# Kernel tuning notes

Measured on AMD Instinct MI355X. Metric: run time of the kernel, lower is better.

The kernel has to match this reference:

```python
import jax, jax.numpy as jnp
import numpy as np

BATCH, T, D_MODEL = 4, 4096, 2048


def setup_inputs() -> dict:
    key = jax.random.key(0)
    kx, ka, kb, kc, kd = jax.random.split(key, 5)
    x = jax.random.normal(kx, (BATCH, T, D_MODEL), dtype=jnp.float32)
    A = jax.random.normal(ka, (D_MODEL,), dtype=jnp.float32)
    B = jax.random.normal(kb, (D_MODEL,), dtype=jnp.float32)
    C = jax.random.normal(kc, (D_MODEL,), dtype=jnp.float32)
    D = jax.random.normal(kd, (D_MODEL,), dtype=jnp.float32)
    return {"x": x, "A": A, "B": B, "C": C, "D": D}


def reference(x, A, B, C, D):
    # Diagonal LTI SSM: h_t = A*h_{t-1} + B*x_t ; y_t = C*h_t + D*x_t
    # x: (batch, T, d_model). Scan over time axis.
    batch, _, d = x.shape
    s0 = jnp.zeros((batch, d), dtype=x.dtype)

    def step(s, xt):
        s = A * s + B * xt          # (batch, d)
        yt = C * s + D * xt
        return s, yt

    # scan over leading axis -> move T to front
    _, ys = jax.lax.scan(step, s0, jnp.swapaxes(x, 0, 1))
    return jnp.swapaxes(ys, 0, 1)   # (batch, T, d_model)
```

## Files before the change

kernel.cpp:

```cpp
#include <hip/hip_runtime.h>

#define BATCHN  4
#define TLEN    4096
#define D4      512
#define DG      8
#define NDG     64
#define THREADS 512
#define TTILE   512
#define NTILE   8
#define NSUB    64
#define TSUB    8
#define TILE_F4 (TTILE * DG)

typedef float f4 __attribute__((ext_vector_type(4)));

__device__ __forceinline__ float fin(float v) {
    return fminf(fmaxf(v, -1.0e30f), 1.0e30f);
}
__device__ __forceinline__ f4 fin4(f4 v) {
    f4 r;
    r.x = fin(v.x); r.y = fin(v.y); r.z = fin(v.z); r.w = fin(v.w);
    return r;
}

struct pr { f4 p, v; };
__device__ __forceinline__ pr comp(pr later, pr earlier) {
    pr r;
    r.p = fin4(later.p * earlier.p);
    r.v = fin4(later.p * earlier.v + later.v);
    return r;
}
__device__ __forceinline__ f4 shflup4(f4 x, int delta) {
    f4 r;
    r.x = __shfl_up(x.x, (unsigned)delta, 64);
    r.y = __shfl_up(x.y, (unsigned)delta, 64);
    r.z = __shfl_up(x.z, (unsigned)delta, 64);
    r.w = __shfl_up(x.w, (unsigned)delta, 64);
    return r;
}

#define BAR() do { asm volatile("s_waitcnt lgkmcnt(0)" ::: "memory"); \
                   __builtin_amdgcn_s_barrier();                       \
                   asm volatile("" ::: "memory"); } while (0)

__device__ __forceinline__ int swz(int row, int col) {
    return row * DG + ((col + (row >> 3)) & 7);
}

__global__ __launch_bounds__(THREADS, 1) void ssm_onepass(
    const float* __restrict__ xg, const float* __restrict__ A,
    const float* __restrict__ B, const float* __restrict__ Cv,
    const float* __restrict__ Dv, float* __restrict__ yg) {
    __shared__ f4 tile[2 * TILE_F4];
    __shared__ f4 wpP[NSUB];
    __shared__ f4 wpV[NSUB];
    __shared__ f4 totP[DG], totV[DG];

    const int tid  = threadIdx.x;
    const int lane = tid & 63;
    const int wid  = tid >> 6;
    const int dg   = blockIdx.x & (NDG - 1);
    const int b    = blockIdx.x >> 6;
    const int ch   = tid & (DG - 1);
    const int sub  = tid >> 3;
    const int siw  = (lane >> 3);

    const int d4 = dg * DG + ch;
    const f4 a  = ((const f4*)A)[d4];
    const f4 bb = ((const f4*)B)[d4];
    const f4 cc = ((const f4*)Cv)[d4];
    const f4 dd = ((const f4*)Dv)[d4];
    const f4 a2 = fin4(a * a), a4 = fin4(a2 * a2), a8 = fin4(a4 * a4);
    const f4 ONE = {1.f, 1.f, 1.f, 1.f};
    const f4 ZERO = {0.f, 0.f, 0.f, 0.f};

    f4 S = ZERO;

    const size_t slice = (size_t)b * TLEN * D4 + (size_t)dg * DG;
    const f4* xbase = (const f4*)xg + slice;
    f4* ybase = (f4*)yg + slice;

    int g_row[TSUB], g_col[TSUB];
#pragma unroll
    for (int q = 0; q < TSUB; ++q) {
        int s = q * THREADS + wid * 64 + lane;
        g_row[q] = s >> 3;
        g_col[q] = ((s & 7) - (s >> 6)) & 7;
    }

#define STAGE(t_, bufi_) do {                                                  \
        const f4* gq;                                                          \
        f4* lq;                                                                \
        _Pragma("unroll")                                                      \
        for (int q = 0; q < TSUB; ++q) {                                       \
            gq = xbase + (size_t)((t_) * TTILE + g_row[q]) * D4 + g_col[q];    \
            lq = &tile[(bufi_) * TILE_F4 + q * THREADS + wid * 64];            \
            __builtin_amdgcn_global_load_lds(                                  \
                (const __attribute__((address_space(1))) void*)gq,             \
                (__attribute__((address_space(3))) void*)lq, 16, 0, 0);        \
        }                                                                      \
    } while (0)

    STAGE(0, 0);
    asm volatile("s_waitcnt vmcnt(0)" ::: "memory");
    __builtin_amdgcn_s_barrier();
    asm volatile("" ::: "memory");

    for (int t = 0; t < NTILE; ++t) {
        f4* bufp = &tile[(t & 1) * TILE_F4];

        if (t + 1 < NTILE) STAGE(t + 1, (t & 1) ^ 1);

        f4 xcur[TSUB];
        const int r0 = sub * TSUB;
#pragma unroll
        for (int i = 0; i < TSUB; ++i) xcur[i] = bufp[swz(r0 + i, ch)];
        pr me;
        {
            f4 v = ZERO;
#pragma unroll
            for (int i = 0; i < TSUB; ++i) v = fin4(a * v + bb * xcur[i]);
            me.p = a8; me.v = v;
        }

#pragma unroll
        for (int d = 1; d <= 4; d <<= 1) {
            pr up;
            up.p = shflup4(me.p, 8 * d);
            up.v = shflup4(me.v, 8 * d);
            if (siw >= d) me = comp(me, up);
        }
        if (siw == 7) { wpP[wid * DG + ch] = me.p; wpV[wid * DG + ch] = me.v; }
        BAR();

        if (tid < 64) {
            const int ww = tid >> 3, c2 = tid & 7;
            pr q; q.p = wpP[tid]; q.v = wpV[tid];
#pragma unroll
            for (int d = 1; d <= 4; d <<= 1) {
                pr up;
                up.p = shflup4(q.p, 8 * d);
                up.v = shflup4(q.v, 8 * d);
                if (ww >= d) q = comp(q, up);
            }
            if (ww == 7) { totP[c2] = q.p; totV[c2] = q.v; }
            pr ex;
            ex.p = shflup4(q.p, 8);
            ex.v = shflup4(q.v, 8);
            if (ww == 0) { ex.p = ONE; ex.v = ZERO; }
            wpP[tid] = ex.p; wpV[tid] = ex.v;
        }
        BAR();

        pr wex; wex.p = wpP[wid * DG + ch]; wex.v = wpV[wid * DG + ch];
        pr mex;
        mex.p = shflup4(me.p, 8);
        mex.v = shflup4(me.v, 8);
        if (siw == 0) { mex.p = ONE; mex.v = ZERO; }
        pr st = comp(mex, wex);
        f4 s = fin4(fin4(st.p * S) + st.v);

        S = fin4(fin4(totP[ch] * S) + totV[ch]);

#pragma unroll
        for (int i = 0; i < TSUB; ++i) {
            f4 xi = xcur[i];
            s = fin4(a * s + bb * xi);
            bufp[swz(r0 + i, ch)] = fin4(cc * s + dd * xi);
        }
        BAR();

#pragma unroll
        for (int q = 0; q < TSUB; ++q) {
            int sIdx = q * THREADS + tid;
            int row = sIdx >> 3;
            int col = ((sIdx & 7) - (sIdx >> 6)) & 7;
            f4 yv = bufp[sIdx];
            __builtin_nontemporal_store(
                yv, ybase + (size_t)(t * TTILE + row) * D4 + col);
        }

        if (t + 1 < NTILE) {
            asm volatile("s_waitcnt vmcnt(8)" ::: "memory");
            __builtin_amdgcn_s_barrier();
            asm volatile("" ::: "memory");
        }
    }
#undef STAGE
}

extern "C" void kernel_launch(void* const* d_in, const int* in_sizes, int n_in,
                              void* d_out, int out_size, void* d_ws, size_t ws_size,
                              hipStream_t stream) {
    const float* x  = (const float*)d_in[0];
    const float* A  = (const float*)d_in[1];
    const float* B  = (const float*)d_in[2];
    const float* Cv = (const float*)d_in[3];
    const float* Dv = (const float*)d_in[4];
    float* y = (float*)d_out;

    const int nblocks = BATCHN * NDG;
    ssm_onepass<<<nblocks, THREADS, 0, stream>>>(x, A, B, Cv, Dv, y);
}
```

Baseline: 53.65 us.

## Load and store directly from global via registers instead of LDS staging

Result: faster. 45.69 us (-14.8%).

```diff
diff --git a/kernel.cpp b/kernel.cpp
--- a/kernel.cpp
+++ b/kernel.cpp
@@ -10,7 +10,6 @@
 #define NTILE   8
 #define NSUB    64
 #define TSUB    8
-#define TILE_F4 (TTILE * DG)
 
 typedef float f4 __attribute__((ext_vector_type(4)));
 
@@ -43,18 +42,12 @@
                    __builtin_amdgcn_s_barrier();                       \
                    asm volatile("" ::: "memory"); } while (0)
 
-__device__ __forceinline__ int swz(int row, int col) {
-    return row * DG + ((col + (row >> 3)) & 7);
-}
-
-__global__ __launch_bounds__(THREADS, 1) void ssm_onepass(
+__global__ __launch_bounds__(THREADS) void ssm_direct(
     const float* __restrict__ xg, const float* __restrict__ A,
     const float* __restrict__ B, const float* __restrict__ Cv,
     const float* __restrict__ Dv, float* __restrict__ yg) {
-    __shared__ f4 tile[2 * TILE_F4];
-    __shared__ f4 wpP[NSUB];
-    __shared__ f4 wpV[NSUB];
-    __shared__ f4 totP[DG], totV[DG];
+    __shared__ f4 wpP[2][NSUB], wpV[2][NSUB];
+    __shared__ f4 totP[2][DG], totV[2][DG];
 
     const int tid  = threadIdx.x;
     const int lane = tid & 63;
@@ -76,45 +69,23 @@
 
     f4 S = ZERO;
 
-    const size_t slice = (size_t)b * TLEN * D4 + (size_t)dg * DG;
-    const f4* xbase = (const f4*)xg + slice;
-    f4* ybase = (f4*)yg + slice;
+    const size_t slice = (size_t)b * TLEN * D4 + (size_t)dg * DG + ch;
+    const f4* xp = (const f4*)xg + slice + (size_t)sub * TSUB * D4;
+    f4* yp = (f4*)yg + slice + (size_t)sub * TSUB * D4;
 
-    int g_row[TSUB], g_col[TSUB];
+    f4 xcur[TSUB], xnext[TSUB];
 #pragma unroll
-    for (int q = 0; q < TSUB; ++q) {
-        int s = q * THREADS + wid * 64 + lane;
-        g_row[q] = s >> 3;
-        g_col[q] = ((s & 7) - (s >> 6)) & 7;
-    }
-
-#define STAGE(t_, bufi_) do {                                                  \
-        const f4* gq;                                                          \
-        f4* lq;                                                                \
-        _Pragma("unroll")                                                      \
-        for (int q = 0; q < TSUB; ++q) {                                       \
-            gq = xbase + (size_t)((t_) * TTILE + g_row[q]) * D4 + g_col[q];    \
-            lq = &tile[(bufi_) * TILE_F4 + q * THREADS + wid * 64];            \
-            __builtin_amdgcn_global_load_lds(                                  \
-                (const __attribute__((address_space(1))) void*)gq,             \
-                (__attribute__((address_space(3))) void*)lq, 16, 0, 0);        \
-        }                                                                      \
-    } while (0)
-
-    STAGE(0, 0);
-    asm volatile("s_waitcnt vmcnt(0)" ::: "memory");
-    __builtin_amdgcn_s_barrier();
-    asm volatile("" ::: "memory");
+    for (int i = 0; i < TSUB; ++i) xcur[i] = xp[(size_t)i * D4];
 
     for (int t = 0; t < NTILE; ++t) {
-        f4* bufp = &tile[(t & 1) * TILE_F4];
+        const int pb = t & 1;
 
-        if (t + 1 < NTILE) STAGE(t + 1, (t & 1) ^ 1);
+        if (t + 1 < NTILE) {
+            const f4* xn = xp + (size_t)(t + 1) * TTILE * D4;
+#pragma unroll
+            for (int i = 0; i < TSUB; ++i) xnext[i] = xn[(size_t)i * D4];
+        }
 
-        f4 xcur[TSUB];
-        const int r0 = sub * TSUB;
-#pragma unroll
-        for (int i = 0; i < TSUB; ++i) xcur[i] = bufp[swz(r0 + i, ch)];
         pr me;
         {
             f4 v = ZERO;
@@ -130,12 +101,12 @@
             up.v = shflup4(me.v, 8 * d);
             if (siw >= d) me = comp(me, up);
         }
-        if (siw == 7) { wpP[wid * DG + ch] = me.p; wpV[wid * DG + ch] = me.v; }
+        if (siw == 7) { wpP[pb][wid * DG + ch] = me.p; wpV[pb][wid * DG + ch] = me.v; }
         BAR();
 
         if (tid < 64) {
             const int ww = tid >> 3, c2 = tid & 7;
-            pr q; q.p = wpP[tid]; q.v = wpV[tid];
+            pr q; q.p = wpP[pb][tid]; q.v = wpV[pb][tid];
 #pragma unroll
             for (int d = 1; d <= 4; d <<= 1) {
                 pr up;
@@ -143,16 +114,16 @@
                 up.v = shflup4(q.v, 8 * d);
                 if (ww >= d) q = comp(q, up);
             }
-            if (ww == 7) { totP[c2] = q.p; totV[c2] = q.v; }
+            if (ww == 7) { totP[pb][c2] = q.p; totV[pb][c2] = q.v; }
             pr ex;
             ex.p = shflup4(q.p, 8);
             ex.v = shflup4(q.v, 8);
             if (ww == 0) { ex.p = ONE; ex.v = ZERO; }
-            wpP[tid] = ex.p; wpV[tid] = ex.v;
+            wpP[pb][tid] = ex.p; wpV[pb][tid] = ex.v;
         }
         BAR();
 
-        pr wex; wex.p = wpP[wid * DG + ch]; wex.v = wpV[wid * DG + ch];
+        pr wex; wex.p = wpP[pb][wid * DG + ch]; wex.v = wpV[pb][wid * DG + ch];
         pr mex;
         mex.p = shflup4(me.p, 8);
         mex.v = shflup4(me.v, 8);
@@ -160,33 +131,22 @@
         pr st = comp(mex, wex);
         f4 s = fin4(fin4(st.p * S) + st.v);
 
-        S = fin4(fin4(totP[ch] * S) + totV[ch]);
+        S = fin4(fin4(totP[pb][ch] * S) + totV[pb][ch]);
 
+        f4* yt = yp + (size_t)t * TTILE * D4;
 #pragma unroll
         for (int i = 0; i < TSUB; ++i) {
             f4 xi = xcur[i];
             s = fin4(a * s + bb * xi);
-            bufp[swz(r0 + i, ch)] = fin4(cc * s + dd * xi);
-        }
-        BAR();
-
-#pragma unroll
-        for (int q = 0; q < TSUB; ++q) {
-            int sIdx = q * THREADS + tid;
-            int row = sIdx >> 3;
-            int col = ((sIdx & 7) - (sIdx >> 6)) & 7;
-            f4 yv = bufp[sIdx];
-            __builtin_nontemporal_store(
-                yv, ybase + (size_t)(t * TTILE + row) * D4 + col);
+            f4 yv = fin4(cc * s + dd * xi);
+            __builtin_nontemporal_store(yv, yt + (size_t)i * D4);
         }
 
         if (t + 1 < NTILE) {
-            asm volatile("s_waitcnt vmcnt(8)" ::: "memory");
-            __builtin_amdgcn_s_barrier();
-            asm volatile("" ::: "memory");
+#pragma unroll
+            for (int i = 0; i < TSUB; ++i) xcur[i] = xnext[i];
         }
     }
-#undef STAGE
 }
 
 extern "C" void kernel_launch(void* const* d_in, const int* in_sizes, int n_in,
@@ -200,5 +160,5 @@
     float* y = (float*)d_out;
 
     const int nblocks = BATCHN * NDG;
-    ssm_onepass<<<nblocks, THREADS, 0, stream>>>(x, A, B, Cv, Dv, y);
+    ssm_direct<<<nblocks, THREADS, 0, stream>>>(x, A, B, Cv, Dv, y);
 }
```
